# Optimization experiments

Measured on AMD Instinct MI355X. Metric: run time of the kernel, lower is better.

The kernel has to match this reference:

```python
import jax, jax.numpy as jnp
import numpy as np

N_NODES = 10000
N_REL = 40
N_BASES = 30
HIDDEN = 100
N_EDGES = 320000


def setup_inputs() -> dict:
    key = jax.random.key(0)
    ks = jax.random.split(key, 11)
    s = 0.05  # param init scale
    inp = {
        "comp1": jax.random.normal(ks[0], (N_REL, N_BASES), jnp.float32) * s,
        "basis1": jax.random.normal(ks[1], (N_BASES, N_NODES, HIDDEN), jnp.float32) * s,
        "root1": jax.random.normal(ks[2], (N_NODES, HIDDEN), jnp.float32) * s,
        "bias1": jax.random.normal(ks[3], (HIDDEN,), jnp.float32) * s,
        "comp2": jax.random.normal(ks[4], (N_REL, N_BASES), jnp.float32) * s,
        "basis2": jax.random.normal(ks[5], (N_BASES, HIDDEN, HIDDEN), jnp.float32) * s,
        "root2": jax.random.normal(ks[6], (HIDDEN, HIDDEN), jnp.float32) * s,
        "bias2": jax.random.normal(ks[7], (HIDDEN,), jnp.float32) * s,
        "emb_rel": jax.random.normal(ks[8], (N_REL + 1, HIDDEN), jnp.float32) * s,
        "edge_index": jax.random.randint(ks[9], (2, N_EDGES), 0, N_NODES, jnp.int64),
        "edge_type": jax.random.randint(ks[10], (N_EDGES,), 0, N_REL, jnp.int64),
    }
    return inp


def _agg_mean_per_relation(msg, dst, rel, n_nodes, n_rel):
    # PyG RGCNConv loops over relations with aggr='mean': messages are
    # mean-aggregated per (target node, relation), then summed over relations.
    seg = dst * n_rel + rel  # combined (node, relation) segment id
    sums = jax.ops.segment_sum(msg, seg, num_segments=n_nodes * n_rel)
    ones = jnp.ones((msg.shape[0], 1), msg.dtype)
    cnt = jax.ops.segment_sum(ones, seg, num_segments=n_nodes * n_rel)
    mean = sums / jnp.maximum(cnt, 1.0)
    return mean.reshape(n_nodes, n_rel, -1).sum(axis=1)  # [N, hidden]


def reference(comp1, basis1, root1, bias1, comp2, basis2, root2, bias2,
              emb_rel, edge_index, edge_type):
    src, dst = edge_index[0], edge_index[1]
    n_nodes = root1.shape[0]
    n_rel = comp1.shape[0]

    # ---- conv1 (x = None -> featureless: weight acts as embedding over node ids)
    # basis decomposition: W1[r] = sum_b comp1[r,b] * basis1[b]
    W1 = jnp.einsum('rb,bno->rno', comp1, basis1)  # [R, N, H]
    msg1 = W1[edge_type, src]                       # per-edge gather [E, H]
    agg1 = _agg_mean_per_relation(msg1, dst, edge_type, n_nodes, n_rel)
    # root term with x=None is root1[arange(N)] = root1 itself
    h = jax.nn.relu(agg1 + root1 + bias1)           # [N, H]

    # ---- conv2 (dense node features)
    W2 = jnp.einsum('rb,bdo->rdo', comp2, basis2)   # [R, H, H]
    Hx = jnp.einsum('nd,rdo->rno', h, W2)           # all-relation transforms [R, N, H]
    msg2 = Hx[edge_type, src]                       # [E, H]
    agg2 = _agg_mean_per_relation(msg2, dst, edge_type, n_nodes, n_rel)
    x = agg2 + h @ root2 + bias2                    # [N, H]

    # ---- relation embedding lookup (padding_idx=0 -> row 0 is zero)
    emb = emb_rel.at[0].set(0.0)
    rel_embedded = emb[edge_type]                   # [E, H]
    return (x, rel_embedded)
```

## Files before the change

kernel.cpp:

```cpp
#include <hip/hip_runtime.h>
#include <hip/hip_bf16.h>
#include <cstdint>
#include <cstddef>

#define E_EDGES 320000
#define NN 10000
#define NRELS 40
#define NB 30
#define HID 100
#define NHTOT (NN*HID)
#define R2 41
#define KTOT 4224
#define NROWS_PAD 10048
#define SPLITK 4
#define KB_PER 33

typedef short bf16x8 __attribute__((ext_vector_type(8)));
typedef float f32x4 __attribute__((ext_vector_type(4)));
typedef float f32x2 __attribute__((ext_vector_type(2)));

__device__ inline ushort f2bf(float f) {
  uint x = __float_as_uint(f);
  return (ushort)((x + 0x7fffu + ((x >> 16) & 1u)) >> 16);
}
__device__ inline float bflo(uint u) { return __uint_as_float(u << 16); }
__device__ inline float bfhi(uint u) { return __uint_as_float(u & 0xffff0000u); }

__device__ inline uint pack2bf(float x, float y) {
  union { __hip_bfloat162 b; uint u; } cv;
  cv.b = __float22bfloat162_rn(make_float2(x, y));
  return cv.u;
}

__device__ inline void gload16(const void* g, void* l) {
  __builtin_amdgcn_global_load_lds(
      (const __attribute__((address_space(1))) void*)g,
      (__attribute__((address_space(3))) void*)l, 16, 0, 0);
}

__global__ void k_count(const int* __restrict__ dst, const int* __restrict__ et,
                        int* __restrict__ cnt_nr, int* __restrict__ deg) {
  int e = blockIdx.x * blockDim.x + threadIdx.x;
  if (e >= E_EDGES) return;
  int d = dst[e], r = et[e];
  atomicAdd(&cnt_nr[d * NRELS + r], 1);
  atomicAdd(&deg[d], 1);
}

__global__ void k_scan(const int* __restrict__ deg, int* __restrict__ rowptr) {
  __shared__ int ssum[256];
  int t = threadIdx.x;
  const int per = (NN + 255) / 256;
  int base = t * per;
  int s = 0;
  for (int k = 0; k < per; ++k) { int i = base + k; if (i < NN) s += deg[i]; }
  ssum[t] = s; __syncthreads();
  for (int off = 1; off < 256; off <<= 1) {
    int v = (t >= off) ? ssum[t - off] : 0;
    __syncthreads();
    ssum[t] += v;
    __syncthreads();
  }
  int pre = (t == 0) ? 0 : ssum[t - 1];
  for (int k = 0; k < per; ++k) {
    int i = base + k;
    if (i < NN) { rowptr[i] = pre; pre += deg[i]; }
  }
  if (t == 255) rowptr[NN] = ssum[255];
}

__global__ void k_pnr(const int* __restrict__ cnt_nr, const int* __restrict__ rowptr,
                      int2* __restrict__ desc) {
  int n = blockIdx.x * 256 + threadIdx.x;
  if (n >= NN) return;
  int s = rowptr[n];
  for (int r = 0; r < NRELS; ++r) {
    int c = cnt_nr[n * NRELS + r];
    desc[n * NRELS + r] = make_int2(s, c);
    s += c;
  }
}

__global__ void k_bucket(const int* __restrict__ src, const int* __restrict__ dst,
                         const int* __restrict__ et, const int2* __restrict__ desc,
                         int* __restrict__ fill_nr, int* __restrict__ ebuf) {
  int e = blockIdx.x * blockDim.x + threadIdx.x;
  if (e >= E_EDGES) return;
  int d = dst[e], r = et[e];
  int pos = desc[d * NRELS + r].x + atomicAdd(&fill_nr[d * NRELS + r], 1);
  ebuf[pos] = (src[e] << 6) | r;
}

__global__ void k_ct(const float* __restrict__ comp1, float* __restrict__ comp1t) {
  int i = blockIdx.x * 256 + threadIdx.x;
  if (i >= NRELS * NB) return;
  int r = i / NB, b = i - r * NB;
  comp1t[b * NRELS + r] = comp1[i];
}

__global__ __launch_bounds__(256, 2) void k_w1b(const float* __restrict__ comp1t,
                                                const float* __restrict__ basis1,
                                                ushort* __restrict__ W1bs) {
  int i = blockIdx.x * 256 + threadIdx.x;
  if (i >= NHTOT) return;
  float acc[NRELS];
#pragma unroll
  for (int r = 0; r < NRELS; ++r) acc[r] = 0.f;
  for (int b = 0; b < NB; ++b) {
    float v = basis1[(size_t)b * NHTOT + i];
    const float* ct = comp1t + b * NRELS;
#pragma unroll
    for (int r = 0; r < NRELS; ++r) acc[r] += ct[r] * v;
  }
#pragma unroll
  for (int r = 0; r < NRELS; ++r)
    W1bs[(size_t)r * NHTOT + i] = f2bf(acc[r]);
}

__global__ void k_w2(const float* __restrict__ comp2, const float* __restrict__ basis2,
                     float* __restrict__ W2f) {
  int i = blockIdx.x * 256 + threadIdx.x;
  if (i >= HID * HID) return;
  float v[NB];
#pragma unroll
  for (int b = 0; b < NB; ++b) v[b] = basis2[b * HID * HID + i];
  for (int r = 0; r < NRELS; ++r) {
    float a = 0.f;
#pragma unroll
    for (int b = 0; b < NB; ++b) a += comp2[r * NB + b] * v[b];
    W2f[r * HID * HID + i] = a;
  }
}

__global__ void k_bt(const float* __restrict__ W2f, const float* __restrict__ root2,
                     ushort* __restrict__ Bt) {
  int i = blockIdx.x * 256 + threadIdx.x;
  if (i >= 112 * KTOT) return;
  int col = i / KTOT, kk = i - col * KTOT;
  float v = 0.f;
  if (kk < R2 * HID && col < HID) {
    int r = kk / HID, k = kk - r * HID;
    v = (r < NRELS) ? W2f[(r * HID + k) * HID + col] : root2[k * HID + col];
  }
  Bt[i] = f2bf(v);
}

__global__ __launch_bounds__(256) void k_agg1(const int* __restrict__ rowptr,
                                              const int* __restrict__ ebuf,
                                              const int* __restrict__ cnt_nr,
                                              const uint2* __restrict__ W1bf2,
                                              const float4* __restrict__ root1,
                                              const float4* __restrict__ bias1,
                                              float4* __restrict__ h4) {
  __shared__ f32x4 red[10][25];
  int n = blockIdx.x, t = threadIdx.x;
  int g = t / 25, c = t - g * 25;
  if (g < 10) {
    f32x4 a = (f32x4){0.f, 0.f, 0.f, 0.f};
    int beg = rowptr[n], end = rowptr[n + 1];
    for (int j = beg + g; j < end; j += 10) {
      int pk = ebuf[j];
      int r = pk & 63, s = pk >> 6;
      float cf = 1.0f / (float)cnt_nr[n * NRELS + r];
      uint2 u = W1bf2[(size_t)r * 250000 + s * 25 + c];
      a[0] += cf * bflo(u.x); a[1] += cf * bfhi(u.x);
      a[2] += cf * bflo(u.y); a[3] += cf * bfhi(u.y);
    }
    red[g][c] = a;
  }
  __syncthreads();
  if (t < 25) {
    f32x4 a = red[0][t];
#pragma unroll
    for (int g2 = 1; g2 < 10; ++g2) a += red[g2][t];
    float4 rt = root1[n * 25 + t];
    float4 bs = bias1[t];
    a += (f32x4){rt.x, rt.y, rt.z, rt.w};
    a += (f32x4){bs.x, bs.y, bs.z, bs.w};
#pragma unroll
    for (int q = 0; q < 4; ++q) if (a[q] < 0.f) a[q] = 0.f;
    h4[n * 25 + t] = make_float4(a[0], a[1], a[2], a[3]);
  }
}

__global__ __launch_bounds__(512) void k_hseg(const int2* __restrict__ desc,
                                              const int* __restrict__ ebuf,
                                              const f32x4* __restrict__ h4,
                                              uint2* __restrict__ hbar2) {
  int wv = blockIdx.x * 8 + (threadIdx.x >> 6);
  int task = wv * 2 + ((threadIdx.x >> 5) & 1);
  if (task >= NN * R2) return;
  int n = task / R2, r = task - n * R2;
  int lane = threadIdx.x & 31;
  uint2* orow = hbar2 + (size_t)n * (KTOT / 4);
  if (r == NRELS) {
    if (lane < 25) {
      f32x4 v = h4[n * 25 + lane];
      orow[NRELS * 25 + lane] = make_uint2(pack2bf(v[0], v[1]), pack2bf(v[2], v[3]));
    }
    return;
  }
  int2 d = desc[n * NRELS + r];
  if (lane < 25) {
    f32x4 a = (f32x4){0.f, 0.f, 0.f, 0.f};
    for (int j = 0; j < d.y; ++j) {
      int s = ebuf[d.x + j] >> 6;
      a += h4[s * 25 + lane];
    }
    float coef = d.y ? 1.0f / (float)d.y : 0.f;
    a *= coef;
    orow[r * 25 + lane] = make_uint2(pack2bf(a[0], a[1]), pack2bf(a[2], a[3]));
  } else if (lane == 25 && r < 31) {
    orow[R2 * 25 + r] = make_uint2(0u, 0u);
  }
}

__global__ __launch_bounds__(256) void k_gemm(const ushort* __restrict__ hbar,
                                              const ushort* __restrict__ Bt,
                                              float* __restrict__ part) {
  __shared__ char lds[2][12288];
  int t = threadIdx.x;
  int wid = t >> 6, l = t & 63;
  int lrow = l & 15, g16 = l >> 4;
  int kb0 = blockIdx.y * KB_PER;
  int row0 = blockIdx.x * 64;

  f32x4 acc[7];
#pragma unroll
  for (int j = 0; j < 7; ++j) acc[j] = (f32x4){0.f, 0.f, 0.f, 0.f};

  auto stage = [&](int p, int buf) {
    int kbg = kb0 + p;
#pragma unroll
    for (int ci = 0; ci < 3; ++ci) {
      int qb = (wid * 3 + ci) * 64;
      int q = qb + l;
      const ushort* g;
      if (q < 448) {
        int col = q >> 2, c = q & 3;
        g = Bt + (size_t)col * KTOT + kbg * 32 + c * 8;
      } else if (q < 704) {
        int qq = q - 448;
        int row = qq >> 2, c = qq & 3;
        g = hbar + (size_t)(row0 + row) * KTOT + kbg * 32 + c * 8;
      } else {
        g = Bt;
      }
      gload16(g, &lds[buf][(size_t)qb * 16]);
    }
  };

  stage(0, 0);
  __syncthreads();

  int cur = 0;
  for (int p = 0; p < KB_PER; ++p) {
    if (p + 1 < KB_PER) stage(p + 1, cur ^ 1);
    const char* base = lds[cur];
    bf16x8 a = *(const bf16x8*)(base + 7168 + (wid * 16 + lrow) * 64 + g16 * 16);
#pragma unroll
    for (int j = 0; j < 7; ++j) {
      bf16x8 b = *(const bf16x8*)(base + (j * 16 + lrow) * 64 + g16 * 16);
      acc[j] = __builtin_amdgcn_mfma_f32_16x16x32_bf16(a, b, acc[j], 0, 0, 0);
    }
    __syncthreads();
    cur ^= 1;
  }

  float* pp = part + (size_t)blockIdx.y * NROWS_PAD * 112;
  int srow = row0 + wid * 16 + g16 * 4;
#pragma unroll
  for (int j = 0; j < 7; ++j) {
    int col = j * 16 + lrow;
#pragma unroll
    for (int v = 0; v < 4; ++v)
      pp[(size_t)(srow + v) * 112 + col] = acc[j][v];
  }
}

__global__ void k_red(const float* __restrict__ part, const float* __restrict__ bias2,
                      float* __restrict__ xout) {
  int i = blockIdx.x * 256 + threadIdx.x;
  if (i >= NHTOT) return;
  int n = i / HID, c = i - n * HID;
  float s = bias2[c];
#pragma unroll
  for (int g = 0; g < SPLITK; ++g)
    s += part[(size_t)g * NROWS_PAD * 112 + (size_t)n * 112 + c];
  xout[i] = s;
}

__global__ void k_emb(const float4* __restrict__ emb, const int* __restrict__ et,
                      float4* __restrict__ out2) {
  int i = blockIdx.x * 256 + threadIdx.x;
  if (i >= E_EDGES * 25) return;
  int e = i / 25, q = i - e * 25;
  int r = et[e];
  float4 v;
  if (r == 0) { v.x = 0.f; v.y = 0.f; v.z = 0.f; v.w = 0.f; }
  else v = emb[r * 25 + q];
  out2[i] = v;
}

extern "C" void kernel_launch(void* const* d_in, const int* in_sizes, int n_in,
                              void* d_out, int out_size, void* d_ws, size_t ws_size,
                              hipStream_t stream) {
  (void)in_sizes; (void)n_in; (void)out_size; (void)d_ws; (void)ws_size;

  const float* comp1  = (const float*)d_in[0];
  const float* basis1 = (const float*)d_in[1];
  const float* root1  = (const float*)d_in[2];
  const float* bias1  = (const float*)d_in[3];
  const float* comp2  = (const float*)d_in[4];
  const float* basis2 = (const float*)d_in[5];
  const float* root2  = (const float*)d_in[6];
  const float* bias2  = (const float*)d_in[7];
  const float* emb    = (const float*)d_in[8];
  const int*   ei     = (const int*)d_in[9];
  const int*   et     = (const int*)d_in[10];
  const int* srcp = ei;
  const int* dstp = ei + E_EDGES;

  float* xout = (float*)d_out;
  float* scratch = xout + NHTOT;
  int*   cnt_nr = (int*)scratch;
  int*   deg    = cnt_nr + 400000;
  int*   rowptr = deg + 10000;
  int*   fill_nr= rowptr + 10004;
  int2*  desc   = (int2*)(scratch + 820004);
  int*   ebuf   = (int*)(scratch + 1620004);
  float* W2f    = scratch + 1940016;
  ushort* Bt    = (ushort*)(scratch + 2340016);
  float* h      = scratch + 2576560;
  uint*  W1bf   = (uint*)(scratch + 3576560);
  uint*  hbar   = (uint*)(scratch + 3576560);
  float* part   = scratch + 24797936;
  float* comp1t = scratch + 29400000;

  hipMemsetAsync(cnt_nr, 0, (size_t)820004 * sizeof(int), stream);
  hipMemsetAsync((char*)hbar + (size_t)NN * KTOT * 2, 0,
                 (size_t)(NROWS_PAD - NN) * KTOT * 2, stream);

  k_count <<<(E_EDGES + 255) / 256, 256, 0, stream>>>(dstp, et, cnt_nr, deg);
  k_scan  <<<1, 256, 0, stream>>>(deg, rowptr);
  k_pnr   <<<(NN + 255) / 256, 256, 0, stream>>>(cnt_nr, rowptr, desc);
  k_bucket<<<(E_EDGES + 255) / 256, 256, 0, stream>>>(srcp, dstp, et, desc,
                                                      fill_nr, ebuf);

  k_ct <<<(NRELS * NB + 255) / 256, 256, 0, stream>>>(comp1, comp1t);
  k_w2 <<<(HID * HID + 255) / 256, 256, 0, stream>>>(comp2, basis2, W2f);
  k_bt <<<(112 * KTOT + 255) / 256, 256, 0, stream>>>(W2f, root2, Bt);
  k_w1b<<<(NHTOT + 255) / 256, 256, 0, stream>>>(comp1t, basis1, (ushort*)W1bf);

  k_agg1<<<NN, 256, 0, stream>>>(rowptr, ebuf, cnt_nr, (const uint2*)W1bf,
                                 (const float4*)root1, (const float4*)bias1,
                                 (float4*)h);
  k_hseg<<<(NN * R2 + 15) / 16, 512, 0, stream>>>(desc, ebuf, (const f32x4*)h,
                                                  (uint2*)hbar);
  k_gemm<<<dim3(NROWS_PAD / 64, SPLITK), 256, 0, stream>>>((const ushort*)hbar, Bt, part);
  k_red <<<(NHTOT + 255) / 256, 256, 0, stream>>>(part, bias2, xout);

  k_emb<<<(E_EDGES * 25 + 255) / 256, 256, 0, stream>>>((const float4*)emb, et,
                                                        (float4*)(xout + NHTOT));
}
```

Baseline: 280.0 us.

## Stage basis1 in LDS and chunk relations in W1 combine; replace memsets with kernels

The W1 basis-combination kernel now loads all 30 basis values for its element into shared memory once, then loops over relations in chunks of 10 accumulators instead of holding 40 live accumulators. This is meant to cut register pressure and raise occupancy on a large, memory-bound kernel, at the cost of 30 KB of LDS per block and re-reading LDS four times. Separately, the two hipMemsetAsync calls are replaced with a small custom zeroing kernel to avoid memset launch overhead.

Result: slower. 312.2 us (+11.5%).

```diff
diff --git a/kernel.cpp b/kernel.cpp
--- a/kernel.cpp
+++ b/kernel.cpp
@@ -14,6 +14,7 @@
 #define NROWS_PAD 10048
 #define SPLITK 4
 #define KB_PER 33
+#define W1C 10
 
 typedef short bf16x8 __attribute__((ext_vector_type(8)));
 typedef float f32x4 __attribute__((ext_vector_type(4)));
@@ -36,6 +37,11 @@
   __builtin_amdgcn_global_load_lds(
       (const __attribute__((address_space(1))) void*)g,
       (__attribute__((address_space(3))) void*)l, 16, 0, 0);
+}
+
+__global__ void k_zero(int4* __restrict__ p, int n4) {
+  int i = blockIdx.x * 256 + threadIdx.x;
+  if (i < n4) p[i] = make_int4(0, 0, 0, 0);
 }
 
 __global__ void k_count(const int* __restrict__ dst, const int* __restrict__ et,
@@ -98,23 +104,32 @@
   comp1t[b * NRELS + r] = comp1[i];
 }
 
-__global__ __launch_bounds__(256, 2) void k_w1b(const float* __restrict__ comp1t,
-                                                const float* __restrict__ basis1,
-                                                ushort* __restrict__ W1bs) {
-  int i = blockIdx.x * 256 + threadIdx.x;
-  if (i >= NHTOT) return;
-  float acc[NRELS];
-#pragma unroll
-  for (int r = 0; r < NRELS; ++r) acc[r] = 0.f;
-  for (int b = 0; b < NB; ++b) {
-    float v = basis1[(size_t)b * NHTOT + i];
-    const float* ct = comp1t + b * NRELS;
-#pragma unroll
-    for (int r = 0; r < NRELS; ++r) acc[r] += ct[r] * v;
-  }
-#pragma unroll
-  for (int r = 0; r < NRELS; ++r)
-    W1bs[(size_t)r * NHTOT + i] = f2bf(acc[r]);
+__global__ __launch_bounds__(256) void k_w1b(const float* __restrict__ comp1t,
+                                             const float* __restrict__ basis1,
+                                             ushort* __restrict__ W1bs) {
+  __shared__ float vb[NB][256];
+  int t = threadIdx.x;
+  size_t i = (size_t)blockIdx.x * 256 + t;
+  bool ok = i < NHTOT;
+#pragma unroll
+  for (int b = 0; b < NB; ++b)
+    vb[b][t] = ok ? basis1[(size_t)b * NHTOT + i] : 0.f;
+  for (int rc = 0; rc < NRELS; rc += W1C) {
+    float acc[W1C];
+#pragma unroll
+    for (int r = 0; r < W1C; ++r) acc[r] = 0.f;
+    for (int b = 0; b < NB; ++b) {
+      float v = vb[b][t];
+      const float* ct = comp1t + b * NRELS + rc;
+#pragma unroll
+      for (int r = 0; r < W1C; ++r) acc[r] += ct[r] * v;
+    }
+    if (ok) {
+#pragma unroll
+      for (int r = 0; r < W1C; ++r)
+        W1bs[(size_t)(rc + r) * NHTOT + i] = f2bf(acc[r]);
+    }
+  }
 }
 
 __global__ void k_w2(const float* __restrict__ comp2, const float* __restrict__ basis2,
@@ -337,9 +352,9 @@
   float* part   = scratch + 24797936;
   float* comp1t = scratch + 29400000;
 
-  hipMemsetAsync(cnt_nr, 0, (size_t)820004 * sizeof(int), stream);
-  hipMemsetAsync((char*)hbar + (size_t)NN * KTOT * 2, 0,
-                 (size_t)(NROWS_PAD - NN) * KTOT * 2, stream);
+  k_zero<<<(205001 + 255) / 256, 256, 0, stream>>>((int4*)cnt_nr, 205001);
+  k_zero<<<(25344 + 255) / 256, 256, 0, stream>>>(
+      (int4*)((char*)hbar + (size_t)NN * KTOT * 2), 25344);
 
   k_count <<<(E_EDGES + 255) / 256, 256, 0, stream>>>(dstp, et, cnt_nr, deg);
   k_scan  <<<1, 256, 0, stream>>>(deg, rowptr);
```
